# Kernel tuning notes

Hardware: AMD Instinct MI355X
Metric: run time of the kernel (lower is better)

Reference implementation:

```python
import jax, jax.numpy as jnp
import numpy as np

B, N, F, H, K, HID, TAB = 4, 256, 1024, 16, 128, 4096, 32
D = F // H
PI = 3.14159  # matches literal in source


def setup_inputs() -> dict:
    key = jax.random.key(0)
    ks = jax.random.split(key, 20)
    r = lambda i, shape: jax.random.normal(ks[i], shape, jnp.float32) * 0.02
    return dict(
        nfeat=jax.random.normal(ks[0], (B, N, F), jnp.float32),
        sp_dist=jax.random.randint(ks[1], (B, N, N), 0, TAB, dtype=jnp.int32),
        rd_dist=jax.random.uniform(ks[2], (B, N, N), jnp.float32),
        dist_table=r(3, (TAB, K)),
        g_means=jax.random.uniform(ks[4], (K,), jnp.float32, 0.0, 3.0),
        g_stds=jax.random.uniform(ks[5], (K,), jnp.float32, 0.0, 3.0),
        g_mul=jnp.ones((1,), jnp.float32),
        g_bias=jnp.zeros((1,), jnp.float32),
        mlp_w1=r(6, (2 * K, H)), mlp_b1=jnp.zeros((H,), jnp.float32),
        mlp_w2=r(7, (H, H)), mlp_b2=jnp.zeros((H,), jnp.float32),
        wq=r(8, (F, F)), bq=jnp.zeros((F,), jnp.float32),
        wk=r(9, (F, F)), bk=jnp.zeros((F,), jnp.float32),
        wv=r(10, (F, F)), bv=jnp.zeros((F,), jnp.float32),
        wo=r(11, (F, F)), bo=jnp.zeros((F,), jnp.float32),
        ffn_w1=r(12, (F, HID)), ffn_b1=jnp.zeros((HID,), jnp.float32),
        ffn_w2=r(13, (HID, F)), ffn_b2=jnp.zeros((F,), jnp.float32),
        ln1_g=jnp.ones((F,), jnp.float32), ln1_b=jnp.zeros((F,), jnp.float32),
        ln2_g=jnp.ones((F,), jnp.float32), ln2_b=jnp.zeros((F,), jnp.float32),
    )


def _layer_norm(x, g, b):
    m = x.mean(-1, keepdims=True)
    v = ((x - m) ** 2).mean(-1, keepdims=True)
    return (x - m) / jnp.sqrt(v + 1e-5) * g + b


def reference(nfeat, sp_dist, rd_dist, dist_table, g_means, g_stds, g_mul, g_bias,
              mlp_w1, mlp_b1, mlp_w2, mlp_b2, wq, bq, wk, bk, wv, bv, wo, bo,
              ffn_w1, ffn_b1, ffn_w2, ffn_b2, ln1_g, ln1_b, ln2_g, ln2_b):
    # --- FusedDistEncoder: shortest-path embedding + Gaussian resistance-distance encoding ---
    sp_emb = dist_table[sp_dist]                      # [B,N,N,K]
    x = g_mul * rd_dist[..., None] + g_bias           # [B,N,N,1] -> broadcast over K
    std = jnp.abs(g_stds) + 0.01                      # [K]
    rd_emb = jnp.exp(-0.5 * ((x - g_means) / std) ** 2) / (((2 * PI) ** 0.5) * std)
    h = jnp.concatenate([sp_emb, rd_emb], axis=-1)    # [B,N,N,2K]
    h = jax.nn.gelu(h @ mlp_w1 + mlp_b1, approximate=False)
    attn_bias = h @ mlp_w2 + mlp_b2                   # [B,N,N,H]

    # --- BiasedMultiheadAttention (note: source divides q by scaling=d^-0.5, i.e. *sqrt(d)) ---
    q = (nfeat @ wq + bq).reshape(B, N, H, D) * (D ** 0.5)
    k = (nfeat @ wk + bk).reshape(B, N, H, D)
    v = (nfeat @ wv + bv).reshape(B, N, H, D)
    scores = jnp.einsum('bihd,bjhd->bijh', q, k) + attn_bias   # [B,N,N,H]
    w = jax.nn.softmax(scores, axis=2)                          # softmax over key dim j
    attn = jnp.einsum('bijh,bjhd->bihd', w, v).reshape(B, N, F) @ wo + bo

    # --- GraphormerLayer residuals (post-norm, dropout=0 / eval) ---
    x1 = _layer_norm(nfeat + attn, ln1_g, ln1_b)
    ffn = jax.nn.relu(x1 @ ffn_w1 + ffn_b1) @ ffn_w2 + ffn_b2
    return _layer_norm(x1 + ffn, ln2_g, ln2_b)
```

## Files before the change

kernel.cpp:

```cpp
#include <hip/hip_runtime.h>
#include <hip/hip_bf16.h>
#include <math.h>

typedef __hip_bfloat16 bf16;
typedef float f32x4 __attribute__((ext_vector_type(4)));
typedef short bf16x8 __attribute__((ext_vector_type(8)));

#define AS1 __attribute__((address_space(1)))
#define AS3 __attribute__((address_space(3)))

__global__ __launch_bounds__(512) void tw_kernel(const float* __restrict__ table,
                                                 const float* __restrict__ w1,
                                                 float* __restrict__ tw) {
    int t = threadIdx.x;
    int r = t >> 4, o = t & 15;
    float a = 0.f;
    for (int k = 0; k < 128; ++k) a += table[r * 128 + k] * w1[k * 16 + o];
    tw[t] = a;
}

__global__ __launch_bounds__(256) void bpack_kernel(const float* __restrict__ bq,
                                                    const float* __restrict__ bk,
                                                    const float* __restrict__ bv,
                                                    float* __restrict__ bqkv) {
    int i = blockIdx.x * 256 + threadIdx.x;
    bqkv[i] = i < 1024 ? bq[i] : (i < 2048 ? bk[i - 1024] : bv[i - 2048]);
}

__global__ __launch_bounds__(256) void cvt_kernel(const float* __restrict__ x,
                                                  bf16* __restrict__ y) {
    int i = (blockIdx.x * 256 + threadIdx.x) * 4;
    float4 v = *reinterpret_cast<const float4*>(x + i);
    y[i + 0] = (bf16)v.x; y[i + 1] = (bf16)v.y;
    y[i + 2] = (bf16)v.z; y[i + 3] = (bf16)v.w;
}

__global__ __launch_bounds__(256) void wt_kernel(const float* __restrict__ W,
                                                 bf16* __restrict__ WT, int Kd, int Nd) {
    __shared__ float tile[32][33];
    int t = threadIdx.x;
    int n0 = blockIdx.x * 32, k0 = blockIdx.y * 32;
    int tx = t & 31, ty = t >> 5;
    #pragma unroll
    for (int p = 0; p < 4; p++)
        tile[ty + p * 8][tx] = W[(k0 + ty + p * 8) * Nd + n0 + tx];
    __syncthreads();
    #pragma unroll
    for (int p = 0; p < 4; p++)
        WT[(n0 + ty + p * 8) * Kd + k0 + tx] = (bf16)tile[tx][ty + p * 8];
}

__global__ __launch_bounds__(256) void enc_kernel(
    const int* __restrict__ sp, const float* __restrict__ rd,
    const float* __restrict__ tw,
    const float* __restrict__ means, const float* __restrict__ stds,
    const float* __restrict__ gmul, const float* __restrict__ gbias,
    const float* __restrict__ w1, const float* __restrict__ b1,
    const float* __restrict__ w2, const float* __restrict__ b2,
    bf16* __restrict__ biasT)
{
    __shared__ float w1s[128][16];
    __shared__ float w2s[16][16];
    __shared__ float b1s[16], b2s[16];
    __shared__ float meanS[128], istdS[128], coefS[128];
    int t = threadIdx.x;
    for (int i = t; i < 2048; i += 256) w1s[i >> 4][i & 15] = w1[2048 + i];
    w2s[t >> 4][t & 15] = w2[t];
    if (t < 16) { b1s[t] = b1[t]; b2s[t] = b2[t]; }
    if (t < 128) {
        float s = fabsf(stds[t]) + 0.01f;
        meanS[t] = means[t];
        istdS[t] = 1.f / s;
        coefS[t] = 1.f / (sqrtf(2.f * 3.14159f) * s);
    }
    __syncthreads();

    int p = blockIdx.x * 256 + t;
    int idx = sp[p];
    float xv = gmul[0] * rd[p] + gbias[0];

    float acc[16];
    #pragma unroll
    for (int o = 0; o < 16; o++) acc[o] = b1s[o] + tw[idx * 16 + o];

    for (int k = 0; k < 128; k++) {
        float d = (xv - meanS[k]) * istdS[k];
        float g = coefS[k] * __expf(-0.5f * d * d);
        #pragma unroll
        for (int o = 0; o < 16; o++) acc[o] += g * w1s[k][o];
    }
    float h[16];
    #pragma unroll
    for (int o = 0; o < 16; o++) {
        float a = acc[o];
        h[o] = 0.5f * a * (1.f + erff(a * 0.70710678118f));
    }
    float outv[16];
    #pragma unroll
    for (int o = 0; o < 16; o++) outv[o] = b2s[o];
    #pragma unroll
    for (int q = 0; q < 16; q++) {
        float hq = h[q];
        #pragma unroll
        for (int o = 0; o < 16; o++) outv[o] += hq * w2s[q][o];
    }
    int b = blockIdx.x >> 8, i = blockIdx.x & 255;
    #pragma unroll
    for (int hh = 0; hh < 16; hh++)
        biasT[(((b * 16 + hh) * 256 + i) << 8) + t] = (bf16)outv[hh];
}

__global__ __launch_bounds__(256, 2) void gemm_bf16(
    const bf16* __restrict__ A, const bf16* __restrict__ BT,
    const float* __restrict__ bias, const float* __restrict__ add,
    void* __restrict__ C, int M, int Nd, int Kd, int epi)
{
    __shared__ __align__(16) char smem[16384];
    int t = threadIdx.x;
    int w = t >> 6, l = t & 63;
    int wr = w >> 1, wc = w & 1;
    int lr = l & 15, hi = l >> 4;
    int row0 = blockIdx.y * 64, col0 = blockIdx.x * 64;
    int nz = gridDim.z;
    int klen = Kd / nz;
    int kbeg = blockIdx.z * klen;

    f32x4 acc[2][2];
    #pragma unroll
    for (int i = 0; i < 2; i++)
        #pragma unroll
        for (int j = 0; j < 2; j++) acc[i][j] = (f32x4){0.f, 0.f, 0.f, 0.f};

    const bf16* Asrc = A + (row0 + (t & 63)) * Kd + kbeg + (t >> 6) * 8;
    const bf16* Bsrc = BT + (col0 + (t & 63)) * Kd + kbeg + (t >> 6) * 8;
    int wbase = (t & 192) * 16;

    int aoff0 = hi * 1024 + (wr * 32 + lr) * 16;
    int boff0 = 4096 + hi * 1024 + (wc * 32 + lr) * 16;

    __builtin_amdgcn_global_load_lds((const AS1 void*)Asrc,
                                     (AS3 void*)(smem + wbase), 16, 0, 0);
    __builtin_amdgcn_global_load_lds((const AS1 void*)Bsrc,
                                     (AS3 void*)(smem + 4096 + wbase), 16, 0, 0);
    __syncthreads();

    int nsteps = klen >> 5;
    int cur = 0;
    for (int s = 0; s < nsteps; ++s) {
        int nxt = cur ^ 1;
        if (s + 1 < nsteps) {
            __builtin_amdgcn_global_load_lds((const AS1 void*)(Asrc + (s + 1) * 32),
                (AS3 void*)(smem + nxt * 8192 + wbase), 16, 0, 0);
            __builtin_amdgcn_global_load_lds((const AS1 void*)(Bsrc + (s + 1) * 32),
                (AS3 void*)(smem + nxt * 8192 + 4096 + wbase), 16, 0, 0);
        }
        const char* base = smem + cur * 8192;
        bf16x8 af[2], bfr[2];
        af[0] = *(const bf16x8*)(base + aoff0);
        af[1] = *(const bf16x8*)(base + aoff0 + 256);
        bfr[0] = *(const bf16x8*)(base + boff0);
        bfr[1] = *(const bf16x8*)(base + boff0 + 256);
        #pragma unroll
        for (int i = 0; i < 2; i++)
            #pragma unroll
            for (int j = 0; j < 2; j++)
                acc[i][j] = __builtin_amdgcn_mfma_f32_16x16x32_bf16(af[i], bfr[j], acc[i][j], 0, 0, 0);
        __syncthreads();
        cur = nxt;
    }

    if (nz > 1) {
        float* P = (float*)C + (size_t)blockIdx.z * M * Nd;
        #pragma unroll
        for (int i = 0; i < 2; i++) {
            int rb = row0 + wr * 32 + i * 16 + hi * 4;
            #pragma unroll
            for (int j = 0; j < 2; j++) {
                int cc = col0 + wc * 32 + j * 16 + lr;
                f32x4 v = acc[i][j];
                #pragma unroll
                for (int q = 0; q < 4; q++) P[(rb + q) * Nd + cc] = v[q];
            }
        }
        return;
    }

    #pragma unroll
    for (int i = 0; i < 2; i++) {
        int rb = row0 + wr * 32 + i * 16 + hi * 4;
        #pragma unroll
        for (int j = 0; j < 2; j++) {
            int cc = col0 + wc * 32 + j * 16 + lr;
            float bsv = bias[cc];
            f32x4 v = acc[i][j];
            #pragma unroll
            for (int q = 0; q < 4; q++) {
                int r = rb + q;
                float x = v[q] + bsv;
                if (epi == 0) {
                    ((float*)C)[r * Nd + cc] = x;
                } else if (epi == 1) {
                    ((float*)C)[r * Nd + cc] = x + add[r * Nd + cc];
                } else if (epi == 2) {
                    ((bf16*)C)[r * Nd + cc] = (bf16)fmaxf(x, 0.f);
                } else {
                    bf16* Cb = (bf16*)C;
                    int sel = cc >> 10, ccc = cc & 1023;
                    int hh = ccc >> 6, dd = ccc & 63;
                    int bb = r >> 8, ii = r & 255;
                    if (sel == 0)
                        Cb[(((bb * 16 + hh) * 256 + ii) << 6) + dd] = (bf16)(x * 8.0f);
                    else if (sel == 1)
                        Cb[1048576 + (((bb * 16 + hh) * 256 + ii) << 6) + dd] = (bf16)x;
                    else
                        Cb[2097152 + ((((bb * 16 + hh) << 6) + dd) << 8) + ii] = (bf16)x;
                }
            }
        }
    }
}

__global__ __launch_bounds__(256) void redadd_kernel(
    const float* __restrict__ part, const float* __restrict__ bias,
    const float* __restrict__ add, float* __restrict__ out, int S)
{
    int i = (blockIdx.x * 256 + threadIdx.x) * 4;
    float4 a = *(const float4*)(part + i);
    for (int s = 1; s < S; s++) {
        float4 b = *(const float4*)(part + s * 1048576 + i);
        a.x += b.x; a.y += b.y; a.z += b.z; a.w += b.w;
    }
    float4 bs = *(const float4*)(bias + (i & 1023));
    float4 ad = *(const float4*)(add + i);
    a.x += bs.x + ad.x; a.y += bs.y + ad.y;
    a.z += bs.z + ad.z; a.w += bs.w + ad.w;
    *(float4*)(out + i) = a;
}

__global__ __launch_bounds__(256) void flash_kernel(
    const bf16* __restrict__ Qb, const bf16* __restrict__ Kb,
    const bf16* __restrict__ VT, const bf16* __restrict__ biasT,
    bf16* __restrict__ out)
{
    __shared__ __align__(16) char pls[32768];
    int t = threadIdx.x;
    int w = t >> 6, l = t & 63;
    int lr = l & 15, hi = l >> 4;
    int bh = blockIdx.x >> 2, iq = blockIdx.x & 3;
    int b = bh >> 4, h = bh & 15;
    int i0 = iq * 64 + w * 16;

    const bf16* Qp = Qb + (bh * 256 + i0 + lr) * 64 + hi * 8;
    bf16x8 qf0 = *(const bf16x8*)(Qp);
    bf16x8 qf1 = *(const bf16x8*)(Qp + 32);

    f32x4 acc[16];
    #pragma unroll
    for (int f = 0; f < 16; f++) acc[f] = (f32x4){0.f, 0.f, 0.f, 0.f};

    const bf16* Kp = Kb + (bh * 256 + lr) * 64 + hi * 8;
    #pragma unroll
    for (int f = 0; f < 16; f++) {
        bf16x8 kf0 = *(const bf16x8*)(Kp + f * 1024);
        bf16x8 kf1 = *(const bf16x8*)(Kp + f * 1024 + 32);
        acc[f] = __builtin_amdgcn_mfma_f32_16x16x32_bf16(qf0, kf0, acc[f], 0, 0, 0);
        acc[f] = __builtin_amdgcn_mfma_f32_16x16x32_bf16(qf1, kf1, acc[f], 0, 0, 0);
    }

    const bf16* bp = biasT + (bh * 256 + i0 + hi * 4) * 256 + lr;
    #pragma unroll
    for (int f = 0; f < 16; f++)
        #pragma unroll
        for (int q = 0; q < 4; q++)
            acc[f][q] += __bfloat162float(bp[q * 256 + f * 16]);

    float inv[4];
    #pragma unroll
    for (int q = 0; q < 4; q++) {
        float m = acc[0][q];
        #pragma unroll
        for (int f = 1; f < 16; f++) m = fmaxf(m, acc[f][q]);
        #pragma unroll
        for (int msk = 1; msk < 16; msk <<= 1) m = fmaxf(m, __shfl_xor(m, msk));
        float s = 0.f;
        #pragma unroll
        for (int f = 0; f < 16; f++) {
            float e = __expf(acc[f][q] - m);
            acc[f][q] = e;
            s += e;
        }
        #pragma unroll
        for (int msk = 1; msk < 16; msk <<= 1) s += __shfl_xor(s, msk);
        inv[q] = 1.f / s;
    }

    char* Pw = pls + w * 8192;
    #pragma unroll
    for (int f = 0; f < 16; f++) {
        int j = f * 16 + lr;
        int c = j >> 3, jo = j & 7;
        #pragma unroll
        for (int q = 0; q < 4; q++)
            *(bf16*)(Pw + c * 256 + (hi * 4 + q) * 16 + jo * 2) = (bf16)(acc[f][q] * inv[q]);
    }
    __syncthreads();

    const char* Pr = pls + w * 8192 + hi * 256 + lr * 16;
    const bf16* Vp = VT + (bh * 64 + lr) * 256 + hi * 8;
    #pragma unroll
    for (int n = 0; n < 4; n++) {
        f32x4 o = (f32x4){0.f, 0.f, 0.f, 0.f};
        #pragma unroll
        for (int ks = 0; ks < 8; ks++) {
            bf16x8 pa = *(const bf16x8*)(Pr + ks * 1024);
            bf16x8 vb = *(const bf16x8*)(Vp + n * 4096 + ks * 32);
            o = __builtin_amdgcn_mfma_f32_16x16x32_bf16(pa, vb, o, 0, 0, 0);
        }
        #pragma unroll
        for (int q = 0; q < 4; q++)
            out[(b * 256 + i0 + hi * 4 + q) * 1024 + h * 64 + n * 16 + lr] = (bf16)o[q];
    }
}

__global__ __launch_bounds__(256) void ln_kernel(
    const float* __restrict__ x, const float* __restrict__ g,
    const float* __restrict__ bta, float* __restrict__ out, bf16* __restrict__ ob)
{
    int row = blockIdx.x;
    int t = threadIdx.x;
    const float* xr = x + row * 1024;
    float v[4];
    float sum = 0.f;
    #pragma unroll
    for (int i = 0; i < 4; i++) { v[i] = xr[t + i * 256]; sum += v[i]; }
    __shared__ float red[8];
    #pragma unroll
    for (int off = 32; off; off >>= 1) sum += __shfl_xor(sum, off);
    if ((t & 63) == 0) red[t >> 6] = sum;
    __syncthreads();
    float mean = (red[0] + red[1] + red[2] + red[3]) * (1.f / 1024.f);
    float vs = 0.f;
    #pragma unroll
    for (int i = 0; i < 4; i++) { float d = v[i] - mean; vs += d * d; }
    #pragma unroll
    for (int off = 32; off; off >>= 1) vs += __shfl_xor(vs, off);
    if ((t & 63) == 0) red[4 + (t >> 6)] = vs;
    __syncthreads();
    float var = (red[4] + red[5] + red[6] + red[7]) * (1.f / 1024.f);
    float invs = rsqrtf(var + 1e-5f);
    #pragma unroll
    for (int i = 0; i < 4; i++) {
        int c = t + i * 256;
        float o = (v[i] - mean) * invs * g[c] + bta[c];
        out[row * 1024 + c] = o;
        if (ob) ob[row * 1024 + c] = (bf16)o;
    }
}

extern "C" void kernel_launch(void* const* d_in, const int* in_sizes, int n_in,
                              void* d_out, int out_size, void* d_ws, size_t ws_size,
                              hipStream_t stream)
{
    const float* nfeat  = (const float*)d_in[0];
    const int*   sp     = (const int*)  d_in[1];
    const float* rd     = (const float*)d_in[2];
    const float* table  = (const float*)d_in[3];
    const float* gmeans = (const float*)d_in[4];
    const float* gstds  = (const float*)d_in[5];
    const float* gmul   = (const float*)d_in[6];
    const float* gbias  = (const float*)d_in[7];
    const float* w1     = (const float*)d_in[8];
    const float* b1     = (const float*)d_in[9];
    const float* w2     = (const float*)d_in[10];
    const float* b2     = (const float*)d_in[11];
    const float* wq     = (const float*)d_in[12];
    const float* bq     = (const float*)d_in[13];
    const float* wk     = (const float*)d_in[14];
    const float* bk     = (const float*)d_in[15];
    const float* wv     = (const float*)d_in[16];
    const float* bv     = (const float*)d_in[17];
    const float* wo     = (const float*)d_in[18];
    const float* bo     = (const float*)d_in[19];
    const float* fw1    = (const float*)d_in[20];
    const float* fb1    = (const float*)d_in[21];
    const float* fw2    = (const float*)d_in[22];
    const float* fb2    = (const float*)d_in[23];
    const float* ln1g   = (const float*)d_in[24];
    const float* ln1b   = (const float*)d_in[25];
    const float* ln2g   = (const float*)d_in[26];
    const float* ln2b   = (const float*)d_in[27];

    const size_t MB = 1 << 20;
    char* cws = (char*)d_ws;
    bf16*  biasT   = (bf16*)(cws);
    bf16*  qkvb    = (bf16*)(cws + 8 * MB);
    float* bqkv    = (float*)(cws + 14 * MB);
    float* tw      = (float*)(cws + 14 * MB + 16384);
    float* part    = (float*)(cws + 16 * MB);
    float* y       = (float*)(cws + 32 * MB);
    float* x1      = (float*)(cws + 36 * MB);
    bf16*  wbuf    = (bf16*)(cws + 40 * MB);
    bf16*  nfeatb  = (bf16*)(cws + 48 * MB);
    bf16*  x1b     = (bf16*)(cws + 50 * MB);
    bf16*  attnob  = (bf16*)(cws + 52 * MB);
    bf16*  hiddenb = biasT;

    tw_kernel<<<1, 512, 0, stream>>>(table, w1, tw);
    bpack_kernel<<<12, 256, 0, stream>>>(bq, bk, bv, bqkv);
    cvt_kernel<<<1024, 256, 0, stream>>>(nfeat, nfeatb);
    enc_kernel<<<1024, 256, 0, stream>>>(sp, rd, tw, gmeans, gstds, gmul, gbias,
                                         w1, b1, w2, b2, biasT);

    wt_kernel<<<dim3(32, 32), 256, 0, stream>>>(wq, wbuf, 1024, 1024);
    wt_kernel<<<dim3(32, 32), 256, 0, stream>>>(wk, wbuf + 1048576, 1024, 1024);
    wt_kernel<<<dim3(32, 32), 256, 0, stream>>>(wv, wbuf + 2097152, 1024, 1024);
    gemm_bf16<<<dim3(48, 16), 256, 0, stream>>>(nfeatb, wbuf, bqkv, nullptr, qkvb,
                                                1024, 3072, 1024, 3);

    flash_kernel<<<256, 256, 0, stream>>>(qkvb, qkvb + 1048576, qkvb + 2097152,
                                          biasT, attnob);

    wt_kernel<<<dim3(32, 32), 256, 0, stream>>>(wo, wbuf, 1024, 1024);
    gemm_bf16<<<dim3(16, 16, 2), 256, 0, stream>>>(attnob, wbuf, bo, nullptr, part,
                                                   1024, 1024, 1024, 0);
    redadd_kernel<<<1024, 256, 0, stream>>>(part, bo, nfeat, y, 2);
    ln_kernel<<<1024, 256, 0, stream>>>(y, ln1g, ln1b, x1, x1b);

    wt_kernel<<<dim3(128, 32), 256, 0, stream>>>(fw1, wbuf, 1024, 4096);
    gemm_bf16<<<dim3(64, 16), 256, 0, stream>>>(x1b, wbuf, fb1, nullptr, hiddenb,
                                                1024, 4096, 1024, 2);

    wt_kernel<<<dim3(32, 128), 256, 0, stream>>>(fw2, wbuf, 4096, 1024);
    gemm_bf16<<<dim3(16, 16, 4), 256, 0, stream>>>(hiddenb, wbuf, fb2, nullptr, part,
                                                   1024, 1024, 4096, 0);
    redadd_kernel<<<1024, 256, 0, stream>>>(part, fb2, x1, y, 4);

    ln_kernel<<<1024, 256, 0, stream>>>(y, ln2g, ln2b, (float*)d_out, nullptr);
}
```

Before: 205.9 us.

## Merge setup and transpose launches, fuse split-K reduce into layernorm, deepen GEMM K-step

Combines the small setup kernels into one launch and does all weight transposes in a single batched kernel. The split-K partial reduction, bias and residual add are folded into the layernorm kernel, so the intermediate y buffer and two launches go away. The GEMM now processes 64 K per stage with 32KB LDS and launch bounds of 4 waves per SIMD, which halves the barrier count. The workspace is re-laid out so part overlaps qkvb, qkvT and woT, relying on those buffers being dead by the time part is written.

Result: faster. 194.8 us (-5.4%).

```diff
diff --git a/kernel.cpp b/kernel.cpp
--- a/kernel.cpp
+++ b/kernel.cpp
@@ -9,37 +9,51 @@
 #define AS1 __attribute__((address_space(1)))
 #define AS3 __attribute__((address_space(3)))
 
-__global__ __launch_bounds__(512) void tw_kernel(const float* __restrict__ table,
-                                                 const float* __restrict__ w1,
-                                                 float* __restrict__ tw) {
-    int t = threadIdx.x;
-    int r = t >> 4, o = t & 15;
-    float a = 0.f;
-    for (int k = 0; k < 128; ++k) a += table[r * 128 + k] * w1[k * 16 + o];
-    tw[t] = a;
-}
-
-__global__ __launch_bounds__(256) void bpack_kernel(const float* __restrict__ bq,
-                                                    const float* __restrict__ bk,
-                                                    const float* __restrict__ bv,
-                                                    float* __restrict__ bqkv) {
-    int i = blockIdx.x * 256 + threadIdx.x;
-    bqkv[i] = i < 1024 ? bq[i] : (i < 2048 ? bk[i - 1024] : bv[i - 2048]);
-}
-
-__global__ __launch_bounds__(256) void cvt_kernel(const float* __restrict__ x,
-                                                  bf16* __restrict__ y) {
-    int i = (blockIdx.x * 256 + threadIdx.x) * 4;
-    float4 v = *reinterpret_cast<const float4*>(x + i);
-    y[i + 0] = (bf16)v.x; y[i + 1] = (bf16)v.y;
-    y[i + 2] = (bf16)v.z; y[i + 3] = (bf16)v.w;
-}
-
-__global__ __launch_bounds__(256) void wt_kernel(const float* __restrict__ W,
-                                                 bf16* __restrict__ WT, int Kd, int Nd) {
+__global__ __launch_bounds__(256) void setup_kernel(
+    const float* __restrict__ nfeat, bf16* __restrict__ nfeatb,
+    const float* __restrict__ bq, const float* __restrict__ bk,
+    const float* __restrict__ bv, float* __restrict__ bqkv,
+    const float* __restrict__ table, const float* __restrict__ w1,
+    float* __restrict__ tw)
+{
+    int bid = blockIdx.x, t = threadIdx.x;
+    if (bid < 1024) {
+        int i = (bid * 256 + t) * 4;
+        float4 v = *reinterpret_cast<const float4*>(nfeat + i);
+        nfeatb[i + 0] = (bf16)v.x; nfeatb[i + 1] = (bf16)v.y;
+        nfeatb[i + 2] = (bf16)v.z; nfeatb[i + 3] = (bf16)v.w;
+    } else if (bid < 1036) {
+        int i = (bid - 1024) * 256 + t;
+        bqkv[i] = i < 1024 ? bq[i] : (i < 2048 ? bk[i - 1024] : bv[i - 2048]);
+    } else {
+        #pragma unroll
+        for (int e = t; e < 512; e += 256) {
+            int r = e >> 4, o = e & 15;
+            float a = 0.f;
+            for (int k = 0; k < 128; ++k) a += table[r * 128 + k] * w1[k * 16 + o];
+            tw[e] = a;
+        }
+    }
+}
+
+__global__ __launch_bounds__(256) void wt_all_kernel(
+    const float* __restrict__ wq, const float* __restrict__ wk,
+    const float* __restrict__ wv, const float* __restrict__ wo,
+    const float* __restrict__ fw1, const float* __restrict__ fw2,
+    bf16* __restrict__ qkvT, bf16* __restrict__ woT,
+    bf16* __restrict__ fw1T, bf16* __restrict__ fw2T)
+{
     __shared__ float tile[32][33];
-    int t = threadIdx.x;
-    int n0 = blockIdx.x * 32, k0 = blockIdx.y * 32;
+    int bid = blockIdx.x, t = threadIdx.x;
+    const float* W; bf16* WT; int Kd, Nd, local;
+    if (bid < 3072)      { int ws = bid >> 10; local = bid & 1023;
+                           W = ws == 0 ? wq : ws == 1 ? wk : wv;
+                           WT = qkvT + ws * 1048576; Kd = 1024; Nd = 1024; }
+    else if (bid < 4096) { local = bid - 3072; W = wo;  WT = woT;  Kd = 1024; Nd = 1024; }
+    else if (bid < 8192) { local = bid - 4096; W = fw1; WT = fw1T; Kd = 1024; Nd = 4096; }
+    else                 { local = bid - 8192; W = fw2; WT = fw2T; Kd = 4096; Nd = 1024; }
+    int ntn = Nd >> 5;
+    int n0 = (local % ntn) * 32, k0 = (local / ntn) * 32;
     int tx = t & 31, ty = t >> 5;
     #pragma unroll
     for (int p = 0; p < 4; p++)
@@ -110,12 +124,12 @@
         biasT[(((b * 16 + hh) * 256 + i) << 8) + t] = (bf16)outv[hh];
 }
 
-__global__ __launch_bounds__(256, 2) void gemm_bf16(
+__global__ __launch_bounds__(256, 4) void gemm_bf16(
     const bf16* __restrict__ A, const bf16* __restrict__ BT,
     const float* __restrict__ bias, const float* __restrict__ add,
     void* __restrict__ C, int M, int Nd, int Kd, int epi)
 {
-    __shared__ __align__(16) char smem[16384];
+    __shared__ __align__(16) char smem[32768];
     int t = threadIdx.x;
     int w = t >> 6, l = t & 63;
     int wr = w >> 1, wc = w & 1;
@@ -135,36 +149,51 @@
     const bf16* Bsrc = BT + (col0 + (t & 63)) * Kd + kbeg + (t >> 6) * 8;
     int wbase = (t & 192) * 16;
 
-    int aoff0 = hi * 1024 + (wr * 32 + lr) * 16;
-    int boff0 = 4096 + hi * 1024 + (wc * 32 + lr) * 16;
-
-    __builtin_amdgcn_global_load_lds((const AS1 void*)Asrc,
-                                     (AS3 void*)(smem + wbase), 16, 0, 0);
-    __builtin_amdgcn_global_load_lds((const AS1 void*)Bsrc,
-                                     (AS3 void*)(smem + 4096 + wbase), 16, 0, 0);
-    __syncthreads();
-
-    int nsteps = klen >> 5;
+    #pragma unroll
+    for (int p = 0; p < 2; p++) {
+        __builtin_amdgcn_global_load_lds((const AS1 void*)(Asrc + p * 32),
+                                         (AS3 void*)(smem + p * 4096 + wbase), 16, 0, 0);
+        __builtin_amdgcn_global_load_lds((const AS1 void*)(Bsrc + p * 32),
+                                         (AS3 void*)(smem + 8192 + p * 4096 + wbase), 16, 0, 0);
+    }
+    __syncthreads();
+
+    int nsteps = klen >> 6;
     int cur = 0;
     for (int s = 0; s < nsteps; ++s) {
         int nxt = cur ^ 1;
         if (s + 1 < nsteps) {
-            __builtin_amdgcn_global_load_lds((const AS1 void*)(Asrc + (s + 1) * 32),
-                (AS3 void*)(smem + nxt * 8192 + wbase), 16, 0, 0);
-            __builtin_amdgcn_global_load_lds((const AS1 void*)(Bsrc + (s + 1) * 32),
-                (AS3 void*)(smem + nxt * 8192 + 4096 + wbase), 16, 0, 0);
-        }
-        const char* base = smem + cur * 8192;
-        bf16x8 af[2], bfr[2];
-        af[0] = *(const bf16x8*)(base + aoff0);
-        af[1] = *(const bf16x8*)(base + aoff0 + 256);
-        bfr[0] = *(const bf16x8*)(base + boff0);
-        bfr[1] = *(const bf16x8*)(base + boff0 + 256);
-        #pragma unroll
-        for (int i = 0; i < 2; i++)
-            #pragma unroll
-            for (int j = 0; j < 2; j++)
-                acc[i][j] = __builtin_amdgcn_mfma_f32_16x16x32_bf16(af[i], bfr[j], acc[i][j], 0, 0, 0);
+            const bf16* An = Asrc + (s + 1) * 64;
+            const bf16* Bn = Bsrc + (s + 1) * 64;
+            #pragma unroll
+            for (int p = 0; p < 2; p++) {
+                __builtin_amdgcn_global_load_lds((const AS1 void*)(An + p * 32),
+                    (AS3 void*)(smem + nxt * 16384 + p * 4096 + wbase), 16, 0, 0);
+                __builtin_amdgcn_global_load_lds((const AS1 void*)(Bn + p * 32),
+                    (AS3 void*)(smem + nxt * 16384 + 8192 + p * 4096 + wbase), 16, 0, 0);
+            }
+        }
+        const char* base = smem + cur * 16384;
+        bf16x8 af[2][2], bfr[2][2];
+        #pragma unroll
+        for (int kk = 0; kk < 2; kk++) {
+            #pragma unroll
+            for (int mi = 0; mi < 2; mi++)
+                af[kk][mi] = *(const bf16x8*)(base + kk * 4096 + hi * 1024 +
+                                              (wr * 32 + mi * 16 + lr) * 16);
+            #pragma unroll
+            for (int nj = 0; nj < 2; nj++)
+                bfr[kk][nj] = *(const bf16x8*)(base + 8192 + kk * 4096 + hi * 1024 +
+                                               (wc * 32 + nj * 16 + lr) * 16);
+        }
+        #pragma unroll
+        for (int kk = 0; kk < 2; kk++)
+            #pragma unroll
+            for (int mi = 0; mi < 2; mi++)
+                #pragma unroll
+                for (int nj = 0; nj < 2; nj++)
+                    acc[mi][nj] = __builtin_amdgcn_mfma_f32_16x16x32_bf16(
+                        af[kk][mi], bfr[kk][nj], acc[mi][nj], 0, 0, 0);
         __syncthreads();
         cur = nxt;
     }
@@ -220,23 +249,6 @@
     }
 }
 
-__global__ __launch_bounds__(256) void redadd_kernel(
-    const float* __restrict__ part, const float* __restrict__ bias,
-    const float* __restrict__ add, float* __restrict__ out, int S)
-{
-    int i = (blockIdx.x * 256 + threadIdx.x) * 4;
-    float4 a = *(const float4*)(part + i);
-    for (int s = 1; s < S; s++) {
-        float4 b = *(const float4*)(part + s * 1048576 + i);
-        a.x += b.x; a.y += b.y; a.z += b.z; a.w += b.w;
-    }
-    float4 bs = *(const float4*)(bias + (i & 1023));
-    float4 ad = *(const float4*)(add + i);
-    a.x += bs.x + ad.x; a.y += bs.y + ad.y;
-    a.z += bs.z + ad.z; a.w += bs.w + ad.w;
-    *(float4*)(out + i) = a;
-}
-
 __global__ __launch_bounds__(256) void flash_kernel(
     const bf16* __restrict__ Qb, const bf16* __restrict__ Kb,
     const bf16* __restrict__ VT, const bf16* __restrict__ biasT,
@@ -322,17 +334,24 @@
     }
 }
 
-__global__ __launch_bounds__(256) void ln_kernel(
-    const float* __restrict__ x, const float* __restrict__ g,
-    const float* __restrict__ bta, float* __restrict__ out, bf16* __restrict__ ob)
+__global__ __launch_bounds__(256) void ln_fused_kernel(
+    const float* __restrict__ part, int S,
+    const float* __restrict__ bias, const float* __restrict__ add,
+    const float* __restrict__ g, const float* __restrict__ bta,
+    float* __restrict__ out, bf16* __restrict__ ob)
 {
     int row = blockIdx.x;
     int t = threadIdx.x;
-    const float* xr = x + row * 1024;
     float v[4];
     float sum = 0.f;
     #pragma unroll
-    for (int i = 0; i < 4; i++) { v[i] = xr[t + i * 256]; sum += v[i]; }
+    for (int i = 0; i < 4; i++) {
+        int c = t + i * 256;
+        float x = add[row * 1024 + c] + bias[c];
+        for (int s = 0; s < S; s++) x += part[s * 1048576 + row * 1024 + c];
+        v[i] = x;
+        sum += x;
+    }
     __shared__ float red[8];
     #pragma unroll
     for (int off = 32; off; off >>= 1) sum += __shfl_xor(sum, off);
@@ -394,46 +413,41 @@
     char* cws = (char*)d_ws;
     bf16*  biasT   = (bf16*)(cws);
     bf16*  qkvb    = (bf16*)(cws + 8 * MB);
-    float* bqkv    = (float*)(cws + 14 * MB);
-    float* tw      = (float*)(cws + 14 * MB + 16384);
-    float* part    = (float*)(cws + 16 * MB);
-    float* y       = (float*)(cws + 32 * MB);
-    float* x1      = (float*)(cws + 36 * MB);
-    bf16*  wbuf    = (bf16*)(cws + 40 * MB);
-    bf16*  nfeatb  = (bf16*)(cws + 48 * MB);
-    bf16*  x1b     = (bf16*)(cws + 50 * MB);
-    bf16*  attnob  = (bf16*)(cws + 52 * MB);
+    float* part    = (float*)(cws + 8 * MB);
+    bf16*  qkvT    = (bf16*)(cws + 16 * MB);
+    bf16*  woT     = (bf16*)(cws + 22 * MB);
+    bf16*  fw1T    = (bf16*)(cws + 24 * MB);
+    bf16*  fw2T    = (bf16*)(cws + 32 * MB);
+    float* x1      = (float*)(cws + 40 * MB);
+    bf16*  nfeatb  = (bf16*)(cws + 44 * MB);
+    bf16*  x1b     = (bf16*)(cws + 46 * MB);
+    bf16*  attnob  = (bf16*)(cws + 48 * MB);
+    float* bqkv    = (float*)(cws + 50 * MB);
+    float* tw      = (float*)(cws + 50 * MB + 16384);
     bf16*  hiddenb = biasT;
 
-    tw_kernel<<<1, 512, 0, stream>>>(table, w1, tw);
-    bpack_kernel<<<12, 256, 0, stream>>>(bq, bk, bv, bqkv);
-    cvt_kernel<<<1024, 256, 0, stream>>>(nfeat, nfeatb);
+    setup_kernel<<<1037, 256, 0, stream>>>(nfeat, nfeatb, bq, bk, bv, bqkv,
+                                           table, w1, tw);
+    wt_all_kernel<<<12288, 256, 0, stream>>>(wq, wk, wv, wo, fw1, fw2,
+                                             qkvT, woT, fw1T, fw2T);
     enc_kernel<<<1024, 256, 0, stream>>>(sp, rd, tw, gmeans, gstds, gmul, gbias,
                                          w1, b1, w2, b2, biasT);
 
-    wt_kernel<<<dim3(32, 32), 256, 0, stream>>>(wq, wbuf, 1024, 1024);
-    wt_kernel<<<dim3(32, 32), 256, 0, stream>>>(wk, wbuf + 1048576, 1024, 1024);
-    wt_kernel<<<dim3(32, 32), 256, 0, stream>>>(wv, wbuf + 2097152, 1024, 1024);
-    gemm_bf16<<<dim3(48, 16), 256, 0, stream>>>(nfeatb, wbuf, bqkv, nullptr, qkvb,
+    gemm_bf16<<<dim3(48, 16), 256, 0, stream>>>(nfeatb, qkvT, bqkv, nullptr, qkvb,
                                                 1024, 3072, 1024, 3);
 
     flash_kernel<<<256, 256, 0, stream>>>(qkvb, qkvb + 1048576, qkvb + 2097152,
                                           biasT, attnob);
 
-    wt_kernel<<<dim3(32, 32), 256, 0, stream>>>(wo, wbuf, 1024, 1024);
-    gemm_bf16<<<dim3(16, 16, 2), 256, 0, stream>>>(attnob, wbuf, bo, nullptr, part,
+    gemm_bf16<<<dim3(16, 16, 2), 256, 0, stream>>>(attnob, woT, bo, nullptr, part,
                                                    1024, 1024, 1024, 0);
-    redadd_kernel<<<1024, 256, 0, stream>>>(part, bo, nfeat, y, 2);
-    ln_kernel<<<1024, 256, 0, stream>>>(y, ln1g, ln1b, x1, x1b);
-
-    wt_kernel<<<dim3(128, 32), 256, 0, stream>>>(fw1, wbuf, 1024, 4096);
-    gemm_bf16<<<dim3(64, 16), 256, 0, stream>>>(x1b, wbuf, fb1, nullptr, hiddenb,
+    ln_fused_kernel<<<1024, 256, 0, stream>>>(part, 2, bo, nfeat, ln1g, ln1b, x1, x1b);
+
+    gemm_bf16<<<dim3(64, 16), 256, 0, stream>>>(x1b, fw1T, fb1, nullptr, hiddenb,
                                                 1024, 4096, 1024, 2);
 
-    wt_kernel<<<dim3(32, 128), 256, 0, stream>>>(fw2, wbuf, 4096, 1024);
-    gemm_bf16<<<dim3(16, 16, 4), 256, 0, stream>>>(hiddenb, wbuf, fb2, nullptr, part,
+    gemm_bf16<<<dim3(16, 16, 4), 256, 0, stream>>>(hiddenb, fw2T, fb2, nullptr, part,
                                                    1024, 1024, 4096, 0);
-    redadd_kernel<<<1024, 256, 0, stream>>>(part, fb2, x1, y, 4);
-
-    ln_kernel<<<1024, 256, 0, stream>>>(y, ln2g, ln2b, (float*)d_out, nullptr);
-}
+    ln_fused_kernel<<<1024, 256, 0, stream>>>(part, 4, fb2, x1, ln2g, ln2b,
+                                              (float*)d_out, nullptr);
+}
```
